# Kernel optimization log

Hardware: AMD Instinct MI355X
Metric: run time of the kernel (lower is better)

## Reference

```python
import jax, jax.numpy as jnp
import numpy as np

S = 1
R = 64
INV_T = 100.0
EVAL_STEPS = 7  # module in eval mode
EPS = 1e-6


def setup_inputs() -> dict:
    key = jax.random.key(0)
    kx, kb = jax.random.split(key)
    B, C, H, W = 8, 512, 64, 64
    x = jax.random.uniform(kx, (B, C, H, W), dtype=jnp.float32)  # non-negative input for NMF
    bases = jax.random.uniform(kb, (B * S, C // S, R), dtype=jnp.float32)
    # F.normalize(bases, dim=1): L2-normalize along D
    bases = bases / jnp.linalg.norm(bases, axis=1, keepdims=True)
    return {"x": x, "bases": bases}


def reference(x, bases):
    B, C, H, W = x.shape
    D = C // S
    N = H * W
    xf = x.reshape(B * S, D, N)  # (BS, D, N)

    # initial coefficients: softmax(inv_t * x^T @ bases)
    coef = jax.nn.softmax(INV_T * jnp.einsum('bdn,bdr->bnr', xf, bases), axis=-1)

    def mu_step(carry, _):
        bases, coef = carry
        # update coef: coef *= (x^T bases) / (coef (bases^T bases) + eps)
        num = jnp.einsum('bdn,bdr->bnr', xf, bases)            # (BS, N, R)
        gram_b = jnp.einsum('bdr,bds->brs', bases, bases)      # (BS, R, R)
        coef = coef * num / (jnp.einsum('bnr,brs->bns', coef, gram_b) + EPS)
        # update bases: bases *= (x coef) / (bases (coef^T coef) + eps)
        num_b = jnp.einsum('bdn,bnr->bdr', xf, coef)           # (BS, D, R)
        gram_c = jnp.einsum('bnr,bns->brs', coef, coef)        # (BS, R, R)
        bases = bases * num_b / (jnp.einsum('bdr,brs->bds', bases, gram_c) + EPS)
        return (bases, coef), None

    (bases, coef), _ = jax.lax.scan(mu_step, (bases, coef), None, length=EVAL_STEPS)

    # compute_coef: one extra coef multiplicative update
    num = jnp.einsum('bdn,bdr->bnr', xf, bases)
    gram_b = jnp.einsum('bdr,bds->brs', bases, bases)
    coef = coef * num / (jnp.einsum('bnr,brs->bns', coef, gram_b) + EPS)

    out = jnp.einsum('bdr,bnr->bdn', bases, coef)  # bases @ coef^T
    return out.reshape(B, C, H, W)
```

## Files before the change

### kernel.cpp

```cpp
#include <hip/hip_runtime.h>
#include <math.h>

#define BATCH 8
#define DD 512
#define NN 4096
#define RR 64
#define NSTEPS 7
#define INV_T 100.0f
#define EPSV 1e-6f
#define GC_SCALE (1.0f / 1024.0f)
#define GC_UNSCALE 1024.0f

typedef __attribute__((ext_vector_type(8))) _Float16 f16x8;
typedef __attribute__((ext_vector_type(4))) _Float16 f16x4;
typedef __attribute__((ext_vector_type(4))) float f32x4;

__device__ __forceinline__ _Float16 f2h(float f) { return (_Float16)f; }

__device__ __forceinline__ void do_xcvt(const float* x, _Float16* x_h,
                                        _Float16* xT_h, int b, int d0, int n0,
                                        int tid, char* smem) {
  _Float16(*t)[72] = (_Float16(*)[72])smem;
  const size_t xbase = (size_t)(b * DD + d0) * NN + n0;
#pragma unroll
  for (int i = 0; i < 4; ++i) {
    const int idx = tid + i * 256;
    const int row = idx >> 4, c4 = (idx & 15) * 4;
    const float4 v = *(const float4*)(x + xbase + (size_t)row * NN + c4);
    f16x4 hv = {f2h(v.x), f2h(v.y), f2h(v.z), f2h(v.w)};
    *(f16x4*)(x_h + xbase + (size_t)row * NN + c4) = hv;
    *(f16x4*)&t[row][c4] = hv;
  }
  __syncthreads();
  const size_t tbase = (size_t)(b * NN + n0) * DD + d0;
#pragma unroll
  for (int i = 0; i < 4; ++i) {
    const int idx = tid + i * 256;
    const int row = idx >> 4, c4 = (idx & 15) * 4;
    f16x4 wv = {t[c4][row], t[c4 + 1][row], t[c4 + 2][row], t[c4 + 3][row]};
    *(f16x4*)(xT_h + tbase + (size_t)row * DD + c4) = wv;
  }
}

__device__ __forceinline__ void do_bases_prep(const float* bin, float* bases32,
                                              _Float16* bases_h,
                                              _Float16* basesT_h, int b, int d0,
                                              int tid, char* smem) {
  float(*t)[65] = (float(*)[65])smem;
  const size_t base = (size_t)(b * DD + d0) * RR;
#pragma unroll
  for (int i = 0; i < 4; ++i) {
    const int idx = tid + i * 256;
    const int row = idx >> 4, c4 = (idx & 15) * 4;
    const float4 v = *(const float4*)(bin + base + row * RR + c4);
    *(float4*)(bases32 + base + row * RR + c4) = v;
    f16x4 hv = {f2h(v.x), f2h(v.y), f2h(v.z), f2h(v.w)};
    *(f16x4*)(bases_h + base + row * RR + c4) = hv;
    t[row][c4] = v.x; t[row][c4 + 1] = v.y; t[row][c4 + 2] = v.z; t[row][c4 + 3] = v.w;
  }
  __syncthreads();
#pragma unroll
  for (int i = 0; i < 4; ++i) {
    const int idx = tid + i * 256;
    const int row = idx >> 4, c4 = (idx & 15) * 4;
    f16x4 wv = {f2h(t[c4][row]), f2h(t[c4 + 1][row]), f2h(t[c4 + 2][row]),
                f2h(t[c4 + 3][row])};
    *(f16x4*)(basesT_h + (size_t)(b * RR + row) * DD + d0 + c4) = wv;
  }
}

__global__ __launch_bounds__(256) void k_gb0(const _Float16* basesT_h,
                                             _Float16* gram_b_h) {
  const int b = blockIdx.x, tid = threadIdx.x;
  const int w = tid >> 6, l = tid & 63, lo = l & 15, hi = l >> 4;
  const _Float16* ap = basesT_h + (size_t)(b * RR + w * 16 + lo) * DD + hi * 8;
  const _Float16* bp = basesT_h + (size_t)(b * RR + lo) * DD + hi * 8;
  f32x4 acc[4] = {};
#pragma unroll
  for (int ks = 0; ks < 16; ++ks) {
    f16x8 a = *(const f16x8*)(ap + ks * 32);
#pragma unroll
    for (int c = 0; c < 4; ++c) {
      f16x8 bb = *(const f16x8*)(bp + (size_t)c * 16 * DD + ks * 32);
      acc[c] = __builtin_amdgcn_mfma_f32_16x16x32_f16(a, bb, acc[c], 0, 0, 0);
    }
  }
  _Float16* op = gram_b_h + (size_t)b * 4096;
#pragma unroll
  for (int c = 0; c < 4; ++c)
#pragma unroll
    for (int r = 0; r < 4; ++r)
      op[(w * 16 + hi * 4 + r) * RR + c * 16 + lo] = f2h(acc[c][r]);
}

__global__ __launch_bounds__(256) void k_gb(const float* pgb,
                                            _Float16* gram_b_h) {
  const int b = blockIdx.x >> 3;
  const int e0 = (blockIdx.x & 7) * 512 + threadIdx.x;
#pragma unroll
  for (int t = 0; t < 2; ++t) {
    const int e = e0 + t * 256;
    float s = 0.f;
#pragma unroll
    for (int sp = 0; sp < 8; ++sp) s += pgb[(size_t)(b * 8 + sp) * 4096 + e];
    gram_b_h[(size_t)b * 4096 + e] = f2h(s);
  }
}

__global__ __launch_bounds__(256) void k_initf(const _Float16* xT_h,
                                               const _Float16* basesT_h,
                                               const _Float16* gram_b_h,
                                               _Float16* coefT_h) {
  __shared__ __attribute__((aligned(16))) _Float16 ct[64][72];
  const int tid = threadIdx.x, w = tid >> 6, l = tid & 63, lo = l & 15,
            hi = l >> 4;
  const int b = blockIdx.x >> 6, n0 = (blockIdx.x & 63) * 64;

  const _Float16* ap = xT_h + (size_t)(b * NN + n0 + w * 16 + lo) * DD + hi * 8;
  const _Float16* bp = basesT_h + (size_t)(b * RR + lo) * DD + hi * 8;
  f32x4 acc[4] = {};
#pragma unroll
  for (int ks = 0; ks < 16; ++ks) {
    f16x8 a = *(const f16x8*)(ap + ks * 32);
#pragma unroll
    for (int c = 0; c < 4; ++c) {
      f16x8 bb = *(const f16x8*)(bp + (size_t)c * 16 * DD + ks * 32);
      acc[c] = __builtin_amdgcn_mfma_f32_16x16x32_f16(a, bb, acc[c], 0, 0, 0);
    }
  }
  float v0[4][4];
#pragma unroll
  for (int reg = 0; reg < 4; ++reg) {
    float m = fmaxf(fmaxf(acc[0][reg], acc[1][reg]),
                    fmaxf(acc[2][reg], acc[3][reg]));
    m = fmaxf(m, __shfl_xor(m, 1));
    m = fmaxf(m, __shfl_xor(m, 2));
    m = fmaxf(m, __shfl_xor(m, 4));
    m = fmaxf(m, __shfl_xor(m, 8));
    float s = 0.f, e[4];
#pragma unroll
    for (int c = 0; c < 4; ++c) {
      e[c] = expf(INV_T * (acc[c][reg] - m));
      s += e[c];
    }
    s += __shfl_xor(s, 1);
    s += __shfl_xor(s, 2);
    s += __shfl_xor(s, 4);
    s += __shfl_xor(s, 8);
    const float inv = 1.f / s;
#pragma unroll
    for (int c = 0; c < 4; ++c) v0[c][reg] = e[c] * inv;
  }
#pragma unroll
  for (int reg = 0; reg < 4; ++reg)
#pragma unroll
    for (int c = 0; c < 4; ++c)
      ct[w * 16 + hi * 4 + reg][c * 16 + lo] = f2h(v0[c][reg]);
  __syncthreads();
  f32x4 den[4] = {};
#pragma unroll
  for (int kk = 0; kk < 2; ++kk) {
    f16x8 a = *(const f16x8*)&ct[w * 16 + lo][kk * 32 + hi * 8];
#pragma unroll
    for (int c = 0; c < 4; ++c) {
      f16x8 gv = *(const f16x8*)(gram_b_h + (size_t)b * 4096 +
                                 (c * 16 + lo) * RR + kk * 32 + hi * 8);
      den[c] = __builtin_amdgcn_mfma_f32_16x16x32_f16(a, gv, den[c], 0, 0, 0);
    }
  }
#pragma unroll
  for (int c = 0; c < 4; ++c) {
    f16x4 t4;
#pragma unroll
    for (int reg = 0; reg < 4; ++reg) {
      const float oldc = (float)ct[w * 16 + hi * 4 + reg][c * 16 + lo];
      t4[reg] = f2h(oldc * acc[c][reg] / (den[c][reg] + EPSV));
    }
    *(f16x4*)(coefT_h + (size_t)(b * RR + c * 16 + lo) * NN + n0 + w * 16 +
              hi * 4) = t4;
  }
}

__device__ __forceinline__ void do_coef1(const _Float16* xT_h,
                                         const _Float16* basesT_h,
                                         const _Float16* gram_b_h,
                                         _Float16* coefT_h, int b, int nt,
                                         int tid, int w, int lo, int hi,
                                         char* smem) {
  _Float16(*ct)[72] = (_Float16(*)[72])smem;
  const int n0 = nt * 64;
#pragma unroll
  for (int i = 0; i < 2; ++i) {
    const int idx = tid + i * 256;
    const int r = idx >> 3, n8 = (idx & 7) * 8;
    f16x8 vv = *(const f16x8*)(coefT_h + (size_t)(b * RR + r) * NN + n0 + n8);
#pragma unroll
    for (int j = 0; j < 8; ++j) ct[n8 + j][r] = vv[j];
  }

  const _Float16* ap = xT_h + (size_t)(b * NN + n0 + w * 16 + lo) * DD + hi * 8;
  const _Float16* bp = basesT_h + (size_t)(b * RR + lo) * DD + hi * 8;
  f32x4 acc[4] = {};
#pragma unroll
  for (int ks = 0; ks < 16; ++ks) {
    f16x8 a = *(const f16x8*)(ap + ks * 32);
#pragma unroll
    for (int c = 0; c < 4; ++c) {
      f16x8 bb = *(const f16x8*)(bp + (size_t)c * 16 * DD + ks * 32);
      acc[c] = __builtin_amdgcn_mfma_f32_16x16x32_f16(a, bb, acc[c], 0, 0, 0);
    }
  }
  __syncthreads();
  f32x4 den[4] = {};
#pragma unroll
  for (int kk = 0; kk < 2; ++kk) {
    f16x8 a = *(const f16x8*)&ct[w * 16 + lo][kk * 32 + hi * 8];
#pragma unroll
    for (int c = 0; c < 4; ++c) {
      f16x8 gv = *(const f16x8*)(gram_b_h + (size_t)b * 4096 +
                                 (c * 16 + lo) * RR + kk * 32 + hi * 8);
      den[c] = __builtin_amdgcn_mfma_f32_16x16x32_f16(a, gv, den[c], 0, 0, 0);
    }
  }
#pragma unroll
  for (int c = 0; c < 4; ++c) {
    f16x4 t4;
#pragma unroll
    for (int reg = 0; reg < 4; ++reg) {
      const float oldc = (float)ct[w * 16 + hi * 4 + reg][c * 16 + lo];
      t4[reg] = f2h(oldc * acc[c][reg] / (den[c][reg] + EPSV));
    }
    *(f16x4*)(coefT_h + (size_t)(b * RR + c * 16 + lo) * NN + n0 + w * 16 +
              hi * 4) = t4;
  }
}

__device__ __forceinline__ void do_numb(const _Float16* x_h,
                                        const _Float16* coefT_h, float* pnb,
                                        int kc, int dt, int b, int w, int lo,
                                        int hi) {
  const _Float16* ap =
      x_h + (size_t)(b * DD + dt * 64 + w * 16 + lo) * NN + kc * 1024 + hi * 8;
  const _Float16* bp = coefT_h + (size_t)(b * RR + lo) * NN + kc * 1024 + hi * 8;
  f32x4 acc[4] = {};
#pragma unroll 4
  for (int ks = 0; ks < 32; ++ks) {
    f16x8 a = *(const f16x8*)(ap + ks * 32);
#pragma unroll
    for (int c = 0; c < 4; ++c) {
      f16x8 bb = *(const f16x8*)(bp + (size_t)c * 16 * NN + ks * 32);
      acc[c] = __builtin_amdgcn_mfma_f32_16x16x32_f16(a, bb, acc[c], 0, 0, 0);
    }
  }
  float* op = pnb + ((size_t)((b * 4 + kc) * DD) + dt * 64 + w * 16 + hi * 4) * RR;
#pragma unroll
  for (int c = 0; c < 4; ++c)
#pragma unroll
    for (int r = 0; r < 4; ++r) op[r * RR + c * 16 + lo] = acc[c][r];
}

__device__ __forceinline__ void do_gramc(const _Float16* coefT_h, float* pgram,
                                         int sp, int b, int w, int lo, int hi) {
  const int k0 = sp * 256;
  const _Float16* ap = coefT_h + (size_t)(b * RR + w * 16 + lo) * NN + k0 + hi * 8;
  const _Float16* bp = coefT_h + (size_t)(b * RR + lo) * NN + k0 + hi * 8;
  f32x4 acc[4] = {};
#pragma unroll
  for (int ks = 0; ks < 8; ++ks) {
    f16x8 a = *(const f16x8*)(ap + ks * 32);
#pragma unroll
    for (int c = 0; c < 4; ++c) {
      f16x8 bb = *(const f16x8*)(bp + (size_t)c * 16 * NN + ks * 32);
      acc[c] = __builtin_amdgcn_mfma_f32_16x16x32_f16(a, bb, acc[c], 0, 0, 0);
    }
  }
  float* op = pgram + ((size_t)(b * 16 + sp) * RR + w * 16 + hi * 4) * RR;
#pragma unroll
  for (int c = 0; c < 4; ++c)
#pragma unroll
    for (int r = 0; r < 4; ++r) op[r * RR + c * 16 + lo] = acc[c][r];
}

__device__ __forceinline__ void do_bases_upd(const float* pnb,
                                             const float* pgram, float* bases32,
                                             _Float16* bases_h,
                                             _Float16* basesT_h, float* pgb,
                                             int dt, int b, int tid, int tx,
                                             int ty, char* smem) {
  float* bsm = (float*)smem;
  _Float16* gsh = (_Float16*)(smem + 16640);
  float* bg = bases32 + (size_t)(b * DD + dt * 64) * RR;
  for (int idx = tid; idx < 4096; idx += 256) {
    const int row = idx >> 6, cc = idx & 63;
    bsm[row * 65 + cc] = bg[row * 64 + cc];
  }
  for (int idx = tid; idx < 4096; idx += 256) {
    float s = 0.f;
#pragma unroll
    for (int sp = 0; sp < 16; ++sp)
      s += pgram[(size_t)(b * 16 + sp) * 4096 + idx];
    gsh[idx] = f2h(s * GC_SCALE);
  }
  __syncthreads();

  float nb[4][4];
#pragma unroll
  for (int i = 0; i < 4; ++i) {
    float4 s = make_float4(0.f, 0.f, 0.f, 0.f);
#pragma unroll
    for (int kc = 0; kc < 4; ++kc) {
      const float4 vv = *(const float4*)(pnb +
          (((size_t)b * 4 + kc) * DD + dt * 64 + ty * 4 + i) * RR + tx * 4);
      s.x += vv.x; s.y += vv.y; s.z += vv.z; s.w += vv.w;
    }
    nb[i][0] = s.x; nb[i][1] = s.y; nb[i][2] = s.z; nb[i][3] = s.w;
  }

  float den[4][4] = {};
  for (int s = 0; s < 64; ++s) {
    float a[4];
#pragma unroll
    for (int i = 0; i < 4; ++i) a[i] = bsm[(ty * 4 + i) * 65 + s];
    const f16x4 gv = *(const f16x4*)&gsh[s * 64 + tx * 4];
    const float g4[4] = {(float)gv[0], (float)gv[1], (float)gv[2], (float)gv[3]};
#pragma unroll
    for (int i = 0; i < 4; ++i)
#pragma unroll
      for (int j = 0; j < 4; ++j) den[i][j] = fmaf(a[i], g4[j], den[i][j]);
  }

  float v[4][4];
#pragma unroll
  for (int i = 0; i < 4; ++i) {
    float4 vv;
#pragma unroll
    for (int j = 0; j < 4; ++j) {
      const float oldb = bsm[(ty * 4 + i) * 65 + tx * 4 + j];
      v[i][j] = oldb * nb[i][j] / fmaf(den[i][j], GC_UNSCALE, EPSV);
    }
    vv.x = v[i][0]; vv.y = v[i][1]; vv.z = v[i][2]; vv.w = v[i][3];
    *(float4*)&bg[(ty * 4 + i) * 64 + tx * 4] = vv;
    f16x4 bv = {f2h(v[i][0]), f2h(v[i][1]), f2h(v[i][2]), f2h(v[i][3])};
    *(f16x4*)(bases_h + (size_t)(b * DD + dt * 64 + ty * 4 + i) * RR + tx * 4) = bv;
  }
#pragma unroll
  for (int j = 0; j < 4; ++j) {
    f16x4 tv = {f2h(v[0][j]), f2h(v[1][j]), f2h(v[2][j]), f2h(v[3][j])};
    *(f16x4*)(basesT_h + (size_t)(b * RR + tx * 4 + j) * DD + dt * 64 + ty * 4) = tv;
  }
  __syncthreads();
#pragma unroll
  for (int i = 0; i < 4; ++i)
#pragma unroll
    for (int j = 0; j < 4; ++j) bsm[(ty * 4 + i) * 65 + tx * 4 + j] = v[i][j];
  __syncthreads();

  float pa[4][4] = {};
  for (int d = 0; d < 64; ++d) {
    float a[4], bb[4];
#pragma unroll
    for (int i = 0; i < 4; ++i) a[i] = bsm[d * 65 + ty * 4 + i];
#pragma unroll
    for (int j = 0; j < 4; ++j) bb[j] = bsm[d * 65 + tx * 4 + j];
#pragma unroll
    for (int i = 0; i < 4; ++i)
#pragma unroll
      for (int j = 0; j < 4; ++j) pa[i][j] = fmaf(a[i], bb[j], pa[i][j]);
  }
  float* pp = pgb + (size_t)(b * 8 + dt) * 4096;
#pragma unroll
  for (int i = 0; i < 4; ++i) {
    float4 vv = make_float4(pa[i][0], pa[i][1], pa[i][2], pa[i][3]);
    *(float4*)(pp + (ty * 4 + i) * 64 + tx * 4) = vv;
  }
}

__global__ __launch_bounds__(256) void k_cout(const _Float16* xT_h,
                                              const _Float16* basesT_h,
                                              const _Float16* gram_b_h,
                                              const _Float16* coefT_h,
                                              const _Float16* bases_h,
                                              float* out) {
  __shared__ __attribute__((aligned(16))) _Float16 ct[64][72];
  const int tid = threadIdx.x, w = tid >> 6, l = tid & 63, lo = l & 15,
            hi = l >> 4;
  const int b = blockIdx.x >> 6, n0 = (blockIdx.x & 63) * 64;

#pragma unroll
  for (int i = 0; i < 2; ++i) {
    const int idx = tid + i * 256;
    const int r = idx >> 3, n8 = (idx & 7) * 8;
    f16x8 vv = *(const f16x8*)(coefT_h + (size_t)(b * RR + r) * NN + n0 + n8);
#pragma unroll
    for (int j = 0; j < 8; ++j) ct[n8 + j][r] = vv[j];
  }

  const _Float16* ap = xT_h + (size_t)(b * NN + n0 + w * 16 + lo) * DD + hi * 8;
  const _Float16* bp = basesT_h + (size_t)(b * RR + lo) * DD + hi * 8;
  f32x4 acc[4] = {};
#pragma unroll
  for (int ks = 0; ks < 16; ++ks) {
    f16x8 a = *(const f16x8*)(ap + ks * 32);
#pragma unroll
    for (int c = 0; c < 4; ++c) {
      f16x8 bb = *(const f16x8*)(bp + (size_t)c * 16 * DD + ks * 32);
      acc[c] = __builtin_amdgcn_mfma_f32_16x16x32_f16(a, bb, acc[c], 0, 0, 0);
    }
  }
  __syncthreads();
  f32x4 den[4] = {};
#pragma unroll
  for (int kk = 0; kk < 2; ++kk) {
    f16x8 a = *(const f16x8*)&ct[w * 16 + lo][kk * 32 + hi * 8];
#pragma unroll
    for (int c = 0; c < 4; ++c) {
      f16x8 gv = *(const f16x8*)(gram_b_h + (size_t)b * 4096 +
                                 (c * 16 + lo) * RR + kk * 32 + hi * 8);
      den[c] = __builtin_amdgcn_mfma_f32_16x16x32_f16(a, gv, den[c], 0, 0, 0);
    }
  }
  float v[4][4];
#pragma unroll
  for (int c = 0; c < 4; ++c)
#pragma unroll
    for (int reg = 0; reg < 4; ++reg) {
      const float oldc = (float)ct[w * 16 + hi * 4 + reg][c * 16 + lo];
      v[c][reg] = oldc * acc[c][reg] / (den[c][reg] + EPSV);
    }
  __syncthreads();
#pragma unroll
  for (int c = 0; c < 4; ++c)
#pragma unroll
    for (int reg = 0; reg < 4; ++reg)
      ct[w * 16 + hi * 4 + reg][c * 16 + lo] = f2h(v[c][reg]);
  __syncthreads();

  for (int dt = 0; dt < 8; ++dt) {
    const _Float16* bap =
        bases_h + (size_t)(b * DD + dt * 64 + w * 16 + lo) * RR + hi * 8;
    f32x4 oacc[4] = {};
#pragma unroll
    for (int kk = 0; kk < 2; ++kk) {
      f16x8 a = *(const f16x8*)(bap + kk * 32);
#pragma unroll
      for (int c = 0; c < 4; ++c) {
        f16x8 bb = *(const f16x8*)&ct[c * 16 + lo][kk * 32 + hi * 8];
        oacc[c] = __builtin_amdgcn_mfma_f32_16x16x32_f16(a, bb, oacc[c], 0, 0, 0);
      }
    }
    float* op = out + (size_t)(b * DD + dt * 64 + w * 16 + hi * 4) * NN + n0;
#pragma unroll
    for (int c = 0; c < 4; ++c)
#pragma unroll
      for (int r = 0; r < 4; ++r) op[(size_t)r * NN + c * 16 + lo] = oacc[c][r];
  }
}

__global__ __launch_bounds__(256) void k_out(const _Float16* bases_h,
                                             const _Float16* coefT_h,
                                             float* out) {
  __shared__ __attribute__((aligned(16))) _Float16 ct[64][72];
  const int tid = threadIdx.x, w = tid >> 6, l = tid & 63, lo = l & 15,
            hi = l >> 4;
  const int nt = blockIdx.x, dt = blockIdx.y, b = blockIdx.z;
  const int n0 = nt * 64;
#pragma unroll
  for (int i = 0; i < 2; ++i) {
    const int idx = tid + i * 256;
    const int r = idx >> 3, n8 = (idx & 7) * 8;
    f16x8 vv = *(const f16x8*)(coefT_h + (size_t)(b * RR + r) * NN + n0 + n8);
#pragma unroll
    for (int j = 0; j < 8; ++j) ct[n8 + j][r] = vv[j];
  }
  __syncthreads();
  const _Float16* ap =
      bases_h + (size_t)(b * DD + dt * 64 + w * 16 + lo) * RR + hi * 8;
  f32x4 acc[4] = {};
#pragma unroll
  for (int kk = 0; kk < 2; ++kk) {
    f16x8 a = *(const f16x8*)(ap + kk * 32);
#pragma unroll
    for (int c = 0; c < 4; ++c) {
      f16x8 bb = *(const f16x8*)&ct[c * 16 + lo][kk * 32 + hi * 8];
      acc[c] = __builtin_amdgcn_mfma_f32_16x16x32_f16(a, bb, acc[c], 0, 0, 0);
    }
  }
  float* op = out + (size_t)(b * DD + dt * 64 + w * 16 + hi * 4) * NN + n0;
#pragma unroll
  for (int c = 0; c < 4; ++c)
#pragma unroll
    for (int r = 0; r < 4; ++r) op[(size_t)r * NN + c * 16 + lo] = acc[c][r];
}

__global__ __launch_bounds__(256) void k_prep(const float* x, const float* bin,
                                              float* b32, _Float16* x_h,
                                              _Float16* xT_h, _Float16* bh,
                                              _Float16* bth) {
  __shared__ __attribute__((aligned(16))) char smem[16640];
  const int g = blockIdx.x, tid = threadIdx.x;
  if (g < 4096)
    do_xcvt(x, x_h, xT_h, g >> 9, ((g >> 6) & 7) * 64, (g & 63) * 64, tid, smem);
  else {
    const int q = g - 4096;
    do_bases_prep(bin, b32, bh, bth, q >> 3, (q & 7) * 64, tid, smem);
  }
}
__global__ __launch_bounds__(256) void k_coef1(const _Float16* xT_h,
                                               const _Float16* basesT_h,
                                               const _Float16* gram_b_h,
                                               _Float16* coefT_h) {
  __shared__ __attribute__((aligned(16))) char smem[9216];
  const int tid = threadIdx.x, w = tid >> 6, l = tid & 63, lo = l & 15,
            hi = l >> 4;
  do_coef1(xT_h, basesT_h, gram_b_h, coefT_h, blockIdx.x >> 6, blockIdx.x & 63,
           tid, w, lo, hi, smem);
}
__global__ __launch_bounds__(256) void k_nbgc(const _Float16* x_h,
                                              const _Float16* coefT_h,
                                              float* pnb, float* pgram) {
  const int tid = threadIdx.x, w = tid >> 6, l = tid & 63, lo = l & 15,
            hi = l >> 4;
  const int g = blockIdx.x;
  if (g < 256)
    do_numb(x_h, coefT_h, pnb, g & 3, (g >> 2) & 7, g >> 5, w, lo, hi);
  else {
    const int q = g - 256;
    do_gramc(coefT_h, pgram, q & 15, q >> 4, w, lo, hi);
  }
}
__global__ __launch_bounds__(256) void k_bupd(const float* pnb,
                                              const float* pgram, float* b32,
                                              _Float16* bh, _Float16* bth,
                                              float* pgb) {
  __shared__ __attribute__((aligned(16))) char smem[24832];
  do_bases_upd(pnb, pgram, b32, bh, bth, pgb, blockIdx.x & 7, blockIdx.x >> 3,
               threadIdx.x, threadIdx.x & 15, threadIdx.x >> 4, smem);
}

extern "C" void kernel_launch(void* const* d_in, const int* in_sizes, int n_in,
                              void* d_out, int out_size, void* d_ws,
                              size_t ws_size, hipStream_t stream) {
  (void)in_sizes; (void)n_in; (void)out_size;
  const float* x = (const float*)d_in[0];
  const float* bin = (const float*)d_in[1];
  float* W = (float*)d_ws;
  float* O = (float*)d_out;

  float* bases32 = W;
  float* pnb = bases32 + 262144;
  float* pgram = pnb + 1048576;
  float* pgb = pgram + 524288;
  _Float16* coefT_h = (_Float16*)(pgb + 262144);
  _Float16* bases_h = coefT_h + 2097152;
  _Float16* basesT_h = bases_h + 262144;
  _Float16* gram_b_h = basesT_h + 262144;
  _Float16* ws_end = gram_b_h + 32768;

  const size_t xhalves = (size_t)BATCH * NN * DD;
  const size_t need = ((char*)(ws_end + 2 * xhalves)) - (char*)W;
  _Float16* xT_h;
  _Float16* x_h;
  const bool ws_fits = (ws_size >= need);
  if (ws_fits) {
    xT_h = ws_end;
    x_h = xT_h + xhalves;
  } else {
    xT_h = (_Float16*)O;
    x_h = xT_h + xhalves;
  }

  k_prep<<<4160, 256, 0, stream>>>(x, bin, bases32, x_h, xT_h, bases_h,
                                   basesT_h);
  k_gb0<<<BATCH, 256, 0, stream>>>(basesT_h, gram_b_h);
  k_initf<<<512, 256, 0, stream>>>(xT_h, basesT_h, gram_b_h, coefT_h);
  for (int s = 0; s < NSTEPS; ++s) {
    k_nbgc<<<384, 256, 0, stream>>>(x_h, coefT_h, pnb, pgram);
    k_bupd<<<64, 256, 0, stream>>>(pnb, pgram, bases32, bases_h, basesT_h, pgb);
    k_gb<<<64, 256, 0, stream>>>(pgb, gram_b_h);
    if (s < NSTEPS - 1)
      k_coef1<<<512, 256, 0, stream>>>(xT_h, basesT_h, gram_b_h, coefT_h);
  }
  if (ws_fits) {
    k_cout<<<512, 256, 0, stream>>>(xT_h, basesT_h, gram_b_h, coefT_h, bases_h,
                                    O);
  } else {
    k_coef1<<<512, 256, 0, stream>>>(xT_h, basesT_h, gram_b_h, coefT_h);
    k_out<<<dim3(64, 8, BATCH), 256, 0, stream>>>(bases_h, coefT_h, O);
  }
}
```

Before: 524.5 us.

## Fuse coef Gram partials into coef-update kernels and interleave batch block mapping

The coefficient Gram matrix (coef^T coef) is now computed per 64-column tile inside k_initf and k_coef1 from the freshly updated coefficients held in shared memory. This removes the separate gram_c blocks that re-read coefT from global memory. As a result k_bupd must reduce 64 partials per batch instead of 16, which it does with float4 loads, and the pgram buffer grows four times. Block indices are also remapped so batch is the fastest-varying dimension, spreading batches across CUs.

```diff
diff --git a/kernel.cpp b/kernel.cpp
--- a/kernel.cpp
+++ b/kernel.cpp
@@ -95,8 +95,8 @@
 
 __global__ __launch_bounds__(256) void k_gb(const float* pgb,
                                             _Float16* gram_b_h) {
-  const int b = blockIdx.x >> 3;
-  const int e0 = (blockIdx.x & 7) * 512 + threadIdx.x;
+  const int b = blockIdx.x & 7;
+  const int e0 = (blockIdx.x >> 3) * 512 + threadIdx.x;
 #pragma unroll
   for (int t = 0; t < 2; ++t) {
     const int e = e0 + t * 256;
@@ -107,14 +107,36 @@
   }
 }
 
+__device__ __forceinline__ void emit_gram(const _Float16 (*ctT)[72],
+                                          float* pgram, int b, int nt, int w,
+                                          int lo, int hi) {
+  f32x4 ga[4] = {};
+#pragma unroll
+  for (int kk = 0; kk < 2; ++kk) {
+    f16x8 a = *(const f16x8*)&ctT[w * 16 + lo][kk * 32 + hi * 8];
+#pragma unroll
+    for (int c = 0; c < 4; ++c) {
+      f16x8 bb = *(const f16x8*)&ctT[c * 16 + lo][kk * 32 + hi * 8];
+      ga[c] = __builtin_amdgcn_mfma_f32_16x16x32_f16(a, bb, ga[c], 0, 0, 0);
+    }
+  }
+  float* gp = pgram + ((size_t)(b * 64 + nt) * RR + w * 16 + hi * 4) * RR;
+#pragma unroll
+  for (int c = 0; c < 4; ++c)
+#pragma unroll
+    for (int r = 0; r < 4; ++r) gp[r * RR + c * 16 + lo] = ga[c][r];
+}
+
 __global__ __launch_bounds__(256) void k_initf(const _Float16* xT_h,
                                                const _Float16* basesT_h,
                                                const _Float16* gram_b_h,
-                                               _Float16* coefT_h) {
+                                               _Float16* coefT_h,
+                                               float* pgram) {
   __shared__ __attribute__((aligned(16))) _Float16 ct[64][72];
+  __shared__ __attribute__((aligned(16))) _Float16 ctT[64][72];
   const int tid = threadIdx.x, w = tid >> 6, l = tid & 63, lo = l & 15,
             hi = l >> 4;
-  const int b = blockIdx.x >> 6, n0 = (blockIdx.x & 63) * 64;
+  const int b = blockIdx.x & 7, nt = blockIdx.x >> 3, n0 = nt * 64;
 
   const _Float16* ap = xT_h + (size_t)(b * NN + n0 + w * 16 + lo) * DD + hi * 8;
   const _Float16* bp = basesT_h + (size_t)(b * RR + lo) * DD + hi * 8;
@@ -174,21 +196,28 @@
 #pragma unroll
     for (int reg = 0; reg < 4; ++reg) {
       const float oldc = (float)ct[w * 16 + hi * 4 + reg][c * 16 + lo];
-      t4[reg] = f2h(oldc * acc[c][reg] / (den[c][reg] + EPSV));
+      const _Float16 nh = f2h(oldc * acc[c][reg] / (den[c][reg] + EPSV));
+      t4[reg] = nh;
+      ctT[c * 16 + lo][w * 16 + hi * 4 + reg] = nh;
     }
     *(f16x4*)(coefT_h + (size_t)(b * RR + c * 16 + lo) * NN + n0 + w * 16 +
               hi * 4) = t4;
   }
-}
-
-__device__ __forceinline__ void do_coef1(const _Float16* xT_h,
-                                         const _Float16* basesT_h,
-                                         const _Float16* gram_b_h,
-                                         _Float16* coefT_h, int b, int nt,
-                                         int tid, int w, int lo, int hi,
-                                         char* smem) {
-  _Float16(*ct)[72] = (_Float16(*)[72])smem;
-  const int n0 = nt * 64;
+  __syncthreads();
+  emit_gram(ctT, pgram, b, nt, w, lo, hi);
+}
+
+__global__ __launch_bounds__(256) void k_coef1(const _Float16* xT_h,
+                                               const _Float16* basesT_h,
+                                               const _Float16* gram_b_h,
+                                               _Float16* coefT_h,
+                                               float* pgram) {
+  __shared__ __attribute__((aligned(16))) _Float16 ct[64][72];
+  __shared__ __attribute__((aligned(16))) _Float16 ctT[64][72];
+  const int tid = threadIdx.x, w = tid >> 6, l = tid & 63, lo = l & 15,
+            hi = l >> 4;
+  const int b = blockIdx.x & 7, nt = blockIdx.x >> 3, n0 = nt * 64;
+
 #pragma unroll
   for (int i = 0; i < 2; ++i) {
     const int idx = tid + i * 256;
@@ -228,17 +257,25 @@
 #pragma unroll
     for (int reg = 0; reg < 4; ++reg) {
       const float oldc = (float)ct[w * 16 + hi * 4 + reg][c * 16 + lo];
-      t4[reg] = f2h(oldc * acc[c][reg] / (den[c][reg] + EPSV));
+      const _Float16 nh = f2h(oldc * acc[c][reg] / (den[c][reg] + EPSV));
+      t4[reg] = nh;
+      ctT[c * 16 + lo][w * 16 + hi * 4 + reg] = nh;
     }
     *(f16x4*)(coefT_h + (size_t)(b * RR + c * 16 + lo) * NN + n0 + w * 16 +
               hi * 4) = t4;
   }
-}
-
-__device__ __forceinline__ void do_numb(const _Float16* x_h,
-                                        const _Float16* coefT_h, float* pnb,
-                                        int kc, int dt, int b, int w, int lo,
-                                        int hi) {
+  __syncthreads();
+  emit_gram(ctT, pgram, b, nt, w, lo, hi);
+}
+
+__global__ __launch_bounds__(256) void k_numb(const _Float16* x_h,
+                                              const _Float16* coefT_h,
+                                              float* pnb) {
+  const int tid = threadIdx.x, w = tid >> 6, l = tid & 63, lo = l & 15,
+            hi = l >> 4;
+  const int b = blockIdx.x & 7;
+  const int q = blockIdx.x >> 3;
+  const int dt = q & 7, kc = q >> 3;
   const _Float16* ap =
       x_h + (size_t)(b * DD + dt * 64 + w * 16 + lo) * NN + kc * 1024 + hi * 8;
   const _Float16* bp = coefT_h + (size_t)(b * RR + lo) * NN + kc * 1024 + hi * 8;
@@ -259,47 +296,32 @@
     for (int r = 0; r < 4; ++r) op[r * RR + c * 16 + lo] = acc[c][r];
 }
 
-__device__ __forceinline__ void do_gramc(const _Float16* coefT_h, float* pgram,
-                                         int sp, int b, int w, int lo, int hi) {
-  const int k0 = sp * 256;
-  const _Float16* ap = coefT_h + (size_t)(b * RR + w * 16 + lo) * NN + k0 + hi * 8;
-  const _Float16* bp = coefT_h + (size_t)(b * RR + lo) * NN + k0 + hi * 8;
-  f32x4 acc[4] = {};
-#pragma unroll
-  for (int ks = 0; ks < 8; ++ks) {
-    f16x8 a = *(const f16x8*)(ap + ks * 32);
-#pragma unroll
-    for (int c = 0; c < 4; ++c) {
-      f16x8 bb = *(const f16x8*)(bp + (size_t)c * 16 * NN + ks * 32);
-      acc[c] = __builtin_amdgcn_mfma_f32_16x16x32_f16(a, bb, acc[c], 0, 0, 0);
-    }
-  }
-  float* op = pgram + ((size_t)(b * 16 + sp) * RR + w * 16 + hi * 4) * RR;
-#pragma unroll
-  for (int c = 0; c < 4; ++c)
-#pragma unroll
-    for (int r = 0; r < 4; ++r) op[r * RR + c * 16 + lo] = acc[c][r];
-}
-
-__device__ __forceinline__ void do_bases_upd(const float* pnb,
-                                             const float* pgram, float* bases32,
-                                             _Float16* bases_h,
-                                             _Float16* basesT_h, float* pgb,
-                                             int dt, int b, int tid, int tx,
-                                             int ty, char* smem) {
+__global__ __launch_bounds__(256) void k_bupd(const float* pnb,
+                                              const float* pgram, float* b32,
+                                              _Float16* bases_h,
+                                              _Float16* basesT_h, float* pgb) {
+  __shared__ __attribute__((aligned(16))) char smem[24832];
   float* bsm = (float*)smem;
   _Float16* gsh = (_Float16*)(smem + 16640);
-  float* bg = bases32 + (size_t)(b * DD + dt * 64) * RR;
+  const int tid = threadIdx.x, tx = tid & 15, ty = tid >> 4;
+  const int b = blockIdx.x & 7, dt = blockIdx.x >> 3;
+  float* bg = b32 + (size_t)(b * DD + dt * 64) * RR;
   for (int idx = tid; idx < 4096; idx += 256) {
     const int row = idx >> 6, cc = idx & 63;
     bsm[row * 65 + cc] = bg[row * 64 + cc];
   }
-  for (int idx = tid; idx < 4096; idx += 256) {
-    float s = 0.f;
-#pragma unroll
-    for (int sp = 0; sp < 16; ++sp)
-      s += pgram[(size_t)(b * 16 + sp) * 4096 + idx];
-    gsh[idx] = f2h(s * GC_SCALE);
+#pragma unroll
+  for (int q = 0; q < 4; ++q) {
+    const int e = q * 1024 + tid * 4;
+    float4 s = make_float4(0.f, 0.f, 0.f, 0.f);
+    for (int sp = 0; sp < 64; ++sp) {
+      const float4 vv = *(const float4*)(pgram + (size_t)(b * 64 + sp) * 4096 + e);
+      s.x += vv.x; s.y += vv.y; s.z += vv.z; s.w += vv.w;
+    }
+    gsh[e + 0] = f2h(s.x * GC_SCALE);
+    gsh[e + 1] = f2h(s.y * GC_SCALE);
+    gsh[e + 2] = f2h(s.z * GC_SCALE);
+    gsh[e + 3] = f2h(s.w * GC_SCALE);
   }
   __syncthreads();
 
@@ -384,7 +406,7 @@
   __shared__ __attribute__((aligned(16))) _Float16 ct[64][72];
   const int tid = threadIdx.x, w = tid >> 6, l = tid & 63, lo = l & 15,
             hi = l >> 4;
-  const int b = blockIdx.x >> 6, n0 = (blockIdx.x & 63) * 64;
+  const int b = blockIdx.x & 7, n0 = (blockIdx.x >> 3) * 64;
 
 #pragma unroll
   for (int i = 0; i < 2; ++i) {
@@ -505,37 +527,6 @@
     do_bases_prep(bin, b32, bh, bth, q >> 3, (q & 7) * 64, tid, smem);
   }
 }
-__global__ __launch_bounds__(256) void k_coef1(const _Float16* xT_h,
-                                               const _Float16* basesT_h,
-                                               const _Float16* gram_b_h,
-                                               _Float16* coefT_h) {
-  __shared__ __attribute__((aligned(16))) char smem[9216];
-  const int tid = threadIdx.x, w = tid >> 6, l = tid & 63, lo = l & 15,
-            hi = l >> 4;
-  do_coef1(xT_h, basesT_h, gram_b_h, coefT_h, blockIdx.x >> 6, blockIdx.x & 63,
-           tid, w, lo, hi, smem);
-}
-__global__ __launch_bounds__(256) void k_nbgc(const _Float16* x_h,
-                                              const _Float16* coefT_h,
-                                              float* pnb, float* pgram) {
-  const int tid = threadIdx.x, w = tid >> 6, l = tid & 63, lo = l & 15,
-            hi = l >> 4;
-  const int g = blockIdx.x;
-  if (g < 256)
-    do_numb(x_h, coefT_h, pnb, g & 3, (g >> 2) & 7, g >> 5, w, lo, hi);
-  else {
-    const int q = g - 256;
-    do_gramc(coefT_h, pgram, q & 15, q >> 4, w, lo, hi);
-  }
-}
-__global__ __launch_bounds__(256) void k_bupd(const float* pnb,
-                                              const float* pgram, float* b32,
-                                              _Float16* bh, _Float16* bth,
-                                              float* pgb) {
-  __shared__ __attribute__((aligned(16))) char smem[24832];
-  do_bases_upd(pnb, pgram, b32, bh, bth, pgb, blockIdx.x & 7, blockIdx.x >> 3,
-               threadIdx.x, threadIdx.x & 15, threadIdx.x >> 4, smem);
-}
 
 extern "C" void kernel_launch(void* const* d_in, const int* in_sizes, int n_in,
                               void* d_out, int out_size, void* d_ws,
@@ -549,7 +540,7 @@
   float* bases32 = W;
   float* pnb = bases32 + 262144;
   float* pgram = pnb + 1048576;
-  float* pgb = pgram + 524288;
+  float* pgb = pgram + 2097152;
   _Float16* coefT_h = (_Float16*)(pgb + 262144);
   _Float16* bases_h = coefT_h + 2097152;
   _Float16* basesT_h = bases_h + 262144;
@@ -572,19 +563,20 @@
   k_prep<<<4160, 256, 0, stream>>>(x, bin, bases32, x_h, xT_h, bases_h,
                                    basesT_h);
   k_gb0<<<BATCH, 256, 0, stream>>>(basesT_h, gram_b_h);
-  k_initf<<<512, 256, 0, stream>>>(xT_h, basesT_h, gram_b_h, coefT_h);
+  k_initf<<<512, 256, 0, stream>>>(xT_h, basesT_h, gram_b_h, coefT_h, pgram);
   for (int s = 0; s < NSTEPS; ++s) {
-    k_nbgc<<<384, 256, 0, stream>>>(x_h, coefT_h, pnb, pgram);
+    k_numb<<<256, 256, 0, stream>>>(x_h, coefT_h, pnb);
     k_bupd<<<64, 256, 0, stream>>>(pnb, pgram, bases32, bases_h, basesT_h, pgb);
     k_gb<<<64, 256, 0, stream>>>(pgb, gram_b_h);
     if (s < NSTEPS - 1)
-      k_coef1<<<512, 256, 0, stream>>>(xT_h, basesT_h, gram_b_h, coefT_h);
+      k_coef1<<<512, 256, 0, stream>>>(xT_h, basesT_h, gram_b_h, coefT_h,
+                                       pgram);
   }
   if (ws_fits) {
     k_cout<<<512, 256, 0, stream>>>(xT_h, basesT_h, gram_b_h, coefT_h, bases_h,
                                     O);
   } else {
-    k_coef1<<<512, 256, 0, stream>>>(xT_h, basesT_h, gram_b_h, coefT_h);
+    k_coef1<<<512, 256, 0, stream>>>(xT_h, basesT_h, gram_b_h, coefT_h, pgram);
     k_out<<<dim3(64, 8, BATCH), 256, 0, stream>>>(bases_h, coefT_h, O);
   }
 }
```

New measurement: 541.6 us. +3.3%, slower.

## Split K across waves and shrink tiles to raise grid parallelism in NMF kernels

Applied to the files above, without the earlier changes.

The coef-update, init and output kernels now work on 32-column tiles, with pairs of waves splitting the 512-long D reduction and combining partial sums through shared memory. This doubles the block count to fill the GPU better. The num_b kernel splits N into 16 chunks instead of 4, giving 1024 blocks plus gram blocks, and the bases update sums more partials from a larger workspace. Block indices are reordered so batch is the fastest-varying index. The trade-offs are extra shared-memory reductions and syncs, half-idle waves in the epilogue, and more partial-sum traffic through global memory.

```diff
diff --git a/kernel.cpp b/kernel.cpp
--- a/kernel.cpp
+++ b/kernel.cpp
@@ -95,8 +95,8 @@
 
 __global__ __launch_bounds__(256) void k_gb(const float* pgb,
                                             _Float16* gram_b_h) {
-  const int b = blockIdx.x >> 3;
-  const int e0 = (blockIdx.x & 7) * 512 + threadIdx.x;
+  const int b = blockIdx.x & 7;
+  const int e0 = (blockIdx.x >> 3) * 512 + threadIdx.x;
 #pragma unroll
   for (int t = 0; t < 2; ++t) {
     const int e = e0 + t * 256;
@@ -111,16 +111,20 @@
                                                const _Float16* basesT_h,
                                                const _Float16* gram_b_h,
                                                _Float16* coefT_h) {
-  __shared__ __attribute__((aligned(16))) _Float16 ct[64][72];
+  __shared__ __attribute__((aligned(16))) float red[16][2][64];
+  __shared__ __attribute__((aligned(16))) _Float16 ct[32][72];
   const int tid = threadIdx.x, w = tid >> 6, l = tid & 63, lo = l & 15,
             hi = l >> 4;
-  const int b = blockIdx.x >> 6, n0 = (blockIdx.x & 63) * 64;
-
-  const _Float16* ap = xT_h + (size_t)(b * NN + n0 + w * 16 + lo) * DD + hi * 8;
-  const _Float16* bp = basesT_h + (size_t)(b * RR + lo) * DD + hi * 8;
+  const int nsub = w >> 1, khalf = w & 1;
+  const int b = blockIdx.x & 7, n0 = (blockIdx.x >> 3) * 32;
+
+  const _Float16* ap = xT_h + (size_t)(b * NN + n0 + nsub * 16 + lo) * DD +
+                       khalf * 256 + hi * 8;
+  const _Float16* bp =
+      basesT_h + (size_t)(b * RR + lo) * DD + khalf * 256 + hi * 8;
   f32x4 acc[4] = {};
 #pragma unroll
-  for (int ks = 0; ks < 16; ++ks) {
+  for (int ks = 0; ks < 8; ++ks) {
     f16x8 a = *(const f16x8*)(ap + ks * 32);
 #pragma unroll
     for (int c = 0; c < 4; ++c) {
@@ -128,81 +132,95 @@
       acc[c] = __builtin_amdgcn_mfma_f32_16x16x32_f16(a, bb, acc[c], 0, 0, 0);
     }
   }
-  float v0[4][4];
-#pragma unroll
-  for (int reg = 0; reg < 4; ++reg) {
-    float m = fmaxf(fmaxf(acc[0][reg], acc[1][reg]),
-                    fmaxf(acc[2][reg], acc[3][reg]));
-    m = fmaxf(m, __shfl_xor(m, 1));
-    m = fmaxf(m, __shfl_xor(m, 2));
-    m = fmaxf(m, __shfl_xor(m, 4));
-    m = fmaxf(m, __shfl_xor(m, 8));
-    float s = 0.f, e[4];
-#pragma unroll
-    for (int c = 0; c < 4; ++c) {
-      e[c] = expf(INV_T * (acc[c][reg] - m));
-      s += e[c];
-    }
-    s += __shfl_xor(s, 1);
-    s += __shfl_xor(s, 2);
-    s += __shfl_xor(s, 4);
-    s += __shfl_xor(s, 8);
-    const float inv = 1.f / s;
-#pragma unroll
-    for (int c = 0; c < 4; ++c) v0[c][reg] = e[c] * inv;
-  }
-#pragma unroll
-  for (int reg = 0; reg < 4; ++reg)
-#pragma unroll
-    for (int c = 0; c < 4; ++c)
-      ct[w * 16 + hi * 4 + reg][c * 16 + lo] = f2h(v0[c][reg]);
-  __syncthreads();
-  f32x4 den[4] = {};
-#pragma unroll
-  for (int kk = 0; kk < 2; ++kk) {
-    f16x8 a = *(const f16x8*)&ct[w * 16 + lo][kk * 32 + hi * 8];
-#pragma unroll
-    for (int c = 0; c < 4; ++c) {
-      f16x8 gv = *(const f16x8*)(gram_b_h + (size_t)b * 4096 +
-                                 (c * 16 + lo) * RR + kk * 32 + hi * 8);
-      den[c] = __builtin_amdgcn_mfma_f32_16x16x32_f16(a, gv, den[c], 0, 0, 0);
-    }
-  }
-#pragma unroll
-  for (int c = 0; c < 4; ++c) {
-    f16x4 t4;
+  if (khalf) {
+#pragma unroll
+    for (int c = 0; c < 4; ++c)
+#pragma unroll
+      for (int reg = 0; reg < 4; ++reg) red[c * 4 + reg][nsub][l] = acc[c][reg];
+  }
+  __syncthreads();
+  if (!khalf) {
+#pragma unroll
+    for (int c = 0; c < 4; ++c)
+#pragma unroll
+      for (int reg = 0; reg < 4; ++reg)
+        acc[c][reg] += red[c * 4 + reg][nsub][l];
 #pragma unroll
     for (int reg = 0; reg < 4; ++reg) {
-      const float oldc = (float)ct[w * 16 + hi * 4 + reg][c * 16 + lo];
-      t4[reg] = f2h(oldc * acc[c][reg] / (den[c][reg] + EPSV));
-    }
-    *(f16x4*)(coefT_h + (size_t)(b * RR + c * 16 + lo) * NN + n0 + w * 16 +
-              hi * 4) = t4;
-  }
-}
-
-__device__ __forceinline__ void do_coef1(const _Float16* xT_h,
-                                         const _Float16* basesT_h,
-                                         const _Float16* gram_b_h,
-                                         _Float16* coefT_h, int b, int nt,
-                                         int tid, int w, int lo, int hi,
-                                         char* smem) {
-  _Float16(*ct)[72] = (_Float16(*)[72])smem;
-  const int n0 = nt * 64;
-#pragma unroll
-  for (int i = 0; i < 2; ++i) {
-    const int idx = tid + i * 256;
-    const int r = idx >> 3, n8 = (idx & 7) * 8;
+      float m = fmaxf(fmaxf(acc[0][reg], acc[1][reg]),
+                      fmaxf(acc[2][reg], acc[3][reg]));
+      m = fmaxf(m, __shfl_xor(m, 1));
+      m = fmaxf(m, __shfl_xor(m, 2));
+      m = fmaxf(m, __shfl_xor(m, 4));
+      m = fmaxf(m, __shfl_xor(m, 8));
+      float s = 0.f, e[4];
+#pragma unroll
+      for (int c = 0; c < 4; ++c) {
+        e[c] = expf(INV_T * (acc[c][reg] - m));
+        s += e[c];
+      }
+      s += __shfl_xor(s, 1);
+      s += __shfl_xor(s, 2);
+      s += __shfl_xor(s, 4);
+      s += __shfl_xor(s, 8);
+      const float inv = 1.f / s;
+#pragma unroll
+      for (int c = 0; c < 4; ++c)
+        ct[nsub * 16 + hi * 4 + reg][c * 16 + lo] = f2h(e[c] * inv);
+    }
+  }
+  __syncthreads();
+  if (!khalf) {
+    f32x4 den[4] = {};
+#pragma unroll
+    for (int kk = 0; kk < 2; ++kk) {
+      f16x8 a = *(const f16x8*)&ct[nsub * 16 + lo][kk * 32 + hi * 8];
+#pragma unroll
+      for (int c = 0; c < 4; ++c) {
+        f16x8 gv = *(const f16x8*)(gram_b_h + (size_t)b * 4096 +
+                                   (c * 16 + lo) * RR + kk * 32 + hi * 8);
+        den[c] = __builtin_amdgcn_mfma_f32_16x16x32_f16(a, gv, den[c], 0, 0, 0);
+      }
+    }
+#pragma unroll
+    for (int c = 0; c < 4; ++c) {
+      f16x4 t4;
+#pragma unroll
+      for (int reg = 0; reg < 4; ++reg) {
+        const float oldc = (float)ct[nsub * 16 + hi * 4 + reg][c * 16 + lo];
+        t4[reg] = f2h(oldc * acc[c][reg] / (den[c][reg] + EPSV));
+      }
+      *(f16x4*)(coefT_h + (size_t)(b * RR + c * 16 + lo) * NN + n0 + nsub * 16 +
+                hi * 4) = t4;
+    }
+  }
+}
+
+__global__ __launch_bounds__(256) void k_coef1(const _Float16* xT_h,
+                                               const _Float16* basesT_h,
+                                               const _Float16* gram_b_h,
+                                               _Float16* coefT_h) {
+  __shared__ __attribute__((aligned(16))) float red[16][2][64];
+  __shared__ __attribute__((aligned(16))) _Float16 ct[32][72];
+  const int tid = threadIdx.x, w = tid >> 6, l = tid & 63, lo = l & 15,
+            hi = l >> 4;
+  const int nsub = w >> 1, khalf = w & 1;
+  const int b = blockIdx.x & 7, n0 = (blockIdx.x >> 3) * 32;
+
+  {
+    const int r = tid >> 2, n8 = (tid & 3) * 8;
     f16x8 vv = *(const f16x8*)(coefT_h + (size_t)(b * RR + r) * NN + n0 + n8);
 #pragma unroll
     for (int j = 0; j < 8; ++j) ct[n8 + j][r] = vv[j];
   }
 
-  const _Float16* ap = xT_h + (size_t)(b * NN + n0 + w * 16 + lo) * DD + hi * 8;
-  const _Float16* bp = basesT_h + (size_t)(b * RR + lo) * DD + hi * 8;
+  const _Float16* ap = xT_h + (size_t)(b * NN + n0 + nsub * 16 + lo) * DD +
+                       khalf * 256 + hi * 8;
+  const _Float16* bp =
+      basesT_h + (size_t)(b * RR + lo) * DD + khalf * 256 + hi * 8;
   f32x4 acc[4] = {};
 #pragma unroll
-  for (int ks = 0; ks < 16; ++ks) {
+  for (int ks = 0; ks < 8; ++ks) {
     f16x8 a = *(const f16x8*)(ap + ks * 32);
 #pragma unroll
     for (int c = 0; c < 4; ++c) {
@@ -210,53 +228,42 @@
       acc[c] = __builtin_amdgcn_mfma_f32_16x16x32_f16(a, bb, acc[c], 0, 0, 0);
     }
   }
-  __syncthreads();
-  f32x4 den[4] = {};
-#pragma unroll
-  for (int kk = 0; kk < 2; ++kk) {
-    f16x8 a = *(const f16x8*)&ct[w * 16 + lo][kk * 32 + hi * 8];
-#pragma unroll
-    for (int c = 0; c < 4; ++c) {
-      f16x8 gv = *(const f16x8*)(gram_b_h + (size_t)b * 4096 +
-                                 (c * 16 + lo) * RR + kk * 32 + hi * 8);
-      den[c] = __builtin_amdgcn_mfma_f32_16x16x32_f16(a, gv, den[c], 0, 0, 0);
-    }
-  }
-#pragma unroll
-  for (int c = 0; c < 4; ++c) {
-    f16x4 t4;
-#pragma unroll
-    for (int reg = 0; reg < 4; ++reg) {
-      const float oldc = (float)ct[w * 16 + hi * 4 + reg][c * 16 + lo];
-      t4[reg] = f2h(oldc * acc[c][reg] / (den[c][reg] + EPSV));
-    }
-    *(f16x4*)(coefT_h + (size_t)(b * RR + c * 16 + lo) * NN + n0 + w * 16 +
-              hi * 4) = t4;
-  }
-}
-
-__device__ __forceinline__ void do_numb(const _Float16* x_h,
-                                        const _Float16* coefT_h, float* pnb,
-                                        int kc, int dt, int b, int w, int lo,
-                                        int hi) {
-  const _Float16* ap =
-      x_h + (size_t)(b * DD + dt * 64 + w * 16 + lo) * NN + kc * 1024 + hi * 8;
-  const _Float16* bp = coefT_h + (size_t)(b * RR + lo) * NN + kc * 1024 + hi * 8;
-  f32x4 acc[4] = {};
-#pragma unroll 4
-  for (int ks = 0; ks < 32; ++ks) {
-    f16x8 a = *(const f16x8*)(ap + ks * 32);
-#pragma unroll
-    for (int c = 0; c < 4; ++c) {
-      f16x8 bb = *(const f16x8*)(bp + (size_t)c * 16 * NN + ks * 32);
-      acc[c] = __builtin_amdgcn_mfma_f32_16x16x32_f16(a, bb, acc[c], 0, 0, 0);
-    }
-  }
-  float* op = pnb + ((size_t)((b * 4 + kc) * DD) + dt * 64 + w * 16 + hi * 4) * RR;
-#pragma unroll
-  for (int c = 0; c < 4; ++c)
-#pragma unroll
-    for (int r = 0; r < 4; ++r) op[r * RR + c * 16 + lo] = acc[c][r];
+  if (khalf) {
+#pragma unroll
+    for (int c = 0; c < 4; ++c)
+#pragma unroll
+      for (int reg = 0; reg < 4; ++reg) red[c * 4 + reg][nsub][l] = acc[c][reg];
+  }
+  __syncthreads();
+  if (!khalf) {
+#pragma unroll
+    for (int c = 0; c < 4; ++c)
+#pragma unroll
+      for (int reg = 0; reg < 4; ++reg)
+        acc[c][reg] += red[c * 4 + reg][nsub][l];
+    f32x4 den[4] = {};
+#pragma unroll
+    for (int kk = 0; kk < 2; ++kk) {
+      f16x8 a = *(const f16x8*)&ct[nsub * 16 + lo][kk * 32 + hi * 8];
+#pragma unroll
+      for (int c = 0; c < 4; ++c) {
+        f16x8 gv = *(const f16x8*)(gram_b_h + (size_t)b * 4096 +
+                                   (c * 16 + lo) * RR + kk * 32 + hi * 8);
+        den[c] = __builtin_amdgcn_mfma_f32_16x16x32_f16(a, gv, den[c], 0, 0, 0);
+      }
+    }
+#pragma unroll
+    for (int c = 0; c < 4; ++c) {
+      f16x4 t4;
+#pragma unroll
+      for (int reg = 0; reg < 4; ++reg) {
+        const float oldc = (float)ct[nsub * 16 + hi * 4 + reg][c * 16 + lo];
+        t4[reg] = f2h(oldc * acc[c][reg] / (den[c][reg] + EPSV));
+      }
+      *(f16x4*)(coefT_h + (size_t)(b * RR + c * 16 + lo) * NN + n0 + nsub * 16 +
+                hi * 4) = t4;
+    }
+  }
 }
 
 __device__ __forceinline__ void do_gramc(const _Float16* coefT_h, float* pgram,
@@ -281,15 +288,51 @@
     for (int r = 0; r < 4; ++r) op[r * RR + c * 16 + lo] = acc[c][r];
 }
 
-__device__ __forceinline__ void do_bases_upd(const float* pnb,
-                                             const float* pgram, float* bases32,
-                                             _Float16* bases_h,
-                                             _Float16* basesT_h, float* pgb,
-                                             int dt, int b, int tid, int tx,
-                                             int ty, char* smem) {
+__global__ __launch_bounds__(256) void k_nbgc(const _Float16* x_h,
+                                              const _Float16* coefT_h,
+                                              float* pnb, float* pgram) {
+  const int tid = threadIdx.x, w = tid >> 6, l = tid & 63, lo = l & 15,
+            hi = l >> 4;
+  const int g = blockIdx.x;
+  if (g < 1024) {
+    const int b = g & 7, q = g >> 3;
+    const int dt = q & 7, kc = q >> 3;
+    const _Float16* ap =
+        x_h + (size_t)(b * DD + dt * 64 + w * 16 + lo) * NN + kc * 256 + hi * 8;
+    const _Float16* bp =
+        coefT_h + (size_t)(b * RR + lo) * NN + kc * 256 + hi * 8;
+    f32x4 acc[4] = {};
+#pragma unroll
+    for (int ks = 0; ks < 8; ++ks) {
+      f16x8 a = *(const f16x8*)(ap + ks * 32);
+#pragma unroll
+      for (int c = 0; c < 4; ++c) {
+        f16x8 bb = *(const f16x8*)(bp + (size_t)c * 16 * NN + ks * 32);
+        acc[c] = __builtin_amdgcn_mfma_f32_16x16x32_f16(a, bb, acc[c], 0, 0, 0);
+      }
+    }
+    float* op =
+        pnb + ((size_t)((b * 16 + kc) * DD) + dt * 64 + w * 16 + hi * 4) * RR;
+#pragma unroll
+    for (int c = 0; c < 4; ++c)
+#pragma unroll
+      for (int r = 0; r < 4; ++r) op[r * RR + c * 16 + lo] = acc[c][r];
+  } else {
+    const int q = g - 1024;
+    do_gramc(coefT_h, pgram, q & 15, q >> 4, w, lo, hi);
+  }
+}
+
+__global__ __launch_bounds__(256) void k_bupd(const float* pnb,
+                                              const float* pgram, float* b32,
+                                              _Float16* bases_h,
+                                              _Float16* basesT_h, float* pgb) {
+  __shared__ __attribute__((aligned(16))) char smem[24832];
   float* bsm = (float*)smem;
   _Float16* gsh = (_Float16*)(smem + 16640);
-  float* bg = bases32 + (size_t)(b * DD + dt * 64) * RR;
+  const int tid = threadIdx.x, tx = tid & 15, ty = tid >> 4;
+  const int b = blockIdx.x & 7, dt = blockIdx.x >> 3;
+  float* bg = b32 + (size_t)(b * DD + dt * 64) * RR;
   for (int idx = tid; idx < 4096; idx += 256) {
     const int row = idx >> 6, cc = idx & 63;
     bsm[row * 65 + cc] = bg[row * 64 + cc];
@@ -308,9 +351,9 @@
   for (int i = 0; i < 4; ++i) {
     float4 s = make_float4(0.f, 0.f, 0.f, 0.f);
 #pragma unroll
-    for (int kc = 0; kc < 4; ++kc) {
+    for (int kc = 0; kc < 16; ++kc) {
       const float4 vv = *(const float4*)(pnb +
-          (((size_t)b * 4 + kc) * DD + dt * 64 + ty * 4 + i) * RR + tx * 4);
+          (((size_t)b * 16 + kc) * DD + dt * 64 + ty * 4 + i) * RR + tx * 4);
       s.x += vv.x; s.y += vv.y; s.z += vv.z; s.w += vv.w;
     }
     nb[i][0] = s.x; nb[i][1] = s.y; nb[i][2] = s.z; nb[i][3] = s.w;
@@ -381,25 +424,27 @@
                                               const _Float16* coefT_h,
                                               const _Float16* bases_h,
                                               float* out) {
-  __shared__ __attribute__((aligned(16))) _Float16 ct[64][72];
+  __shared__ __attribute__((aligned(16))) float red[16][2][64];
+  __shared__ __attribute__((aligned(16))) _Float16 ct[32][72];
   const int tid = threadIdx.x, w = tid >> 6, l = tid & 63, lo = l & 15,
             hi = l >> 4;
-  const int b = blockIdx.x >> 6, n0 = (blockIdx.x & 63) * 64;
-
-#pragma unroll
-  for (int i = 0; i < 2; ++i) {
-    const int idx = tid + i * 256;
-    const int r = idx >> 3, n8 = (idx & 7) * 8;
+  const int nsub = w >> 1, khalf = w & 1;
+  const int b = blockIdx.x & 7, n0 = (blockIdx.x >> 3) * 32;
+
+  {
+    const int r = tid >> 2, n8 = (tid & 3) * 8;
     f16x8 vv = *(const f16x8*)(coefT_h + (size_t)(b * RR + r) * NN + n0 + n8);
 #pragma unroll
     for (int j = 0; j < 8; ++j) ct[n8 + j][r] = vv[j];
   }
 
-  const _Float16* ap = xT_h + (size_t)(b * NN + n0 + w * 16 + lo) * DD + hi * 8;
-  const _Float16* bp = basesT_h + (size_t)(b * RR + lo) * DD + hi * 8;
+  const _Float16* ap = xT_h + (size_t)(b * NN + n0 + nsub * 16 + lo) * DD +
+                       khalf * 256 + hi * 8;
+  const _Float16* bp =
+      basesT_h + (size_t)(b * RR + lo) * DD + khalf * 256 + hi * 8;
   f32x4 acc[4] = {};
 #pragma unroll
-  for (int ks = 0; ks < 16; ++ks) {
+  for (int ks = 0; ks < 8; ++ks) {
     f16x8 a = *(const f16x8*)(ap + ks * 32);
 #pragma unroll
     for (int c = 0; c < 4; ++c) {
@@ -407,50 +452,57 @@
       acc[c] = __builtin_amdgcn_mfma_f32_16x16x32_f16(a, bb, acc[c], 0, 0, 0);
     }
   }
-  __syncthreads();
-  f32x4 den[4] = {};
-#pragma unroll
-  for (int kk = 0; kk < 2; ++kk) {
-    f16x8 a = *(const f16x8*)&ct[w * 16 + lo][kk * 32 + hi * 8];
-#pragma unroll
-    for (int c = 0; c < 4; ++c) {
-      f16x8 gv = *(const f16x8*)(gram_b_h + (size_t)b * 4096 +
-                                 (c * 16 + lo) * RR + kk * 32 + hi * 8);
-      den[c] = __builtin_amdgcn_mfma_f32_16x16x32_f16(a, gv, den[c], 0, 0, 0);
-    }
-  }
-  float v[4][4];
-#pragma unroll
-  for (int c = 0; c < 4; ++c)
-#pragma unroll
-    for (int reg = 0; reg < 4; ++reg) {
-      const float oldc = (float)ct[w * 16 + hi * 4 + reg][c * 16 + lo];
-      v[c][reg] = oldc * acc[c][reg] / (den[c][reg] + EPSV);
-    }
-  __syncthreads();
-#pragma unroll
-  for (int c = 0; c < 4; ++c)
-#pragma unroll
-    for (int reg = 0; reg < 4; ++reg)
-      ct[w * 16 + hi * 4 + reg][c * 16 + lo] = f2h(v[c][reg]);
+  if (khalf) {
+#pragma unroll
+    for (int c = 0; c < 4; ++c)
+#pragma unroll
+      for (int reg = 0; reg < 4; ++reg) red[c * 4 + reg][nsub][l] = acc[c][reg];
+  }
+  __syncthreads();
+  if (!khalf) {
+#pragma unroll
+    for (int c = 0; c < 4; ++c)
+#pragma unroll
+      for (int reg = 0; reg < 4; ++reg)
+        acc[c][reg] += red[c * 4 + reg][nsub][l];
+    f32x4 den[4] = {};
+#pragma unroll
+    for (int kk = 0; kk < 2; ++kk) {
+      f16x8 a = *(const f16x8*)&ct[nsub * 16 + lo][kk * 32 + hi * 8];
+#pragma unroll
+      for (int c = 0; c < 4; ++c) {
+        f16x8 gv = *(const f16x8*)(gram_b_h + (size_t)b * 4096 +
+                                   (c * 16 + lo) * RR + kk * 32 + hi * 8);
+        den[c] = __builtin_amdgcn_mfma_f32_16x16x32_f16(a, gv, den[c], 0, 0, 0);
+      }
+    }
+#pragma unroll
+    for (int c = 0; c < 4; ++c)
+#pragma unroll
+      for (int reg = 0; reg < 4; ++reg) {
+        const float oldc = (float)ct[nsub * 16 + hi * 4 + reg][c * 16 + lo];
+        ct[nsub * 16 + hi * 4 + reg][c * 16 + lo] =
+            f2h(oldc * acc[c][reg] / (den[c][reg] + EPSV));
+      }
+  }
   __syncthreads();
 
   for (int dt = 0; dt < 8; ++dt) {
     const _Float16* bap =
         bases_h + (size_t)(b * DD + dt * 64 + w * 16 + lo) * RR + hi * 8;
-    f32x4 oacc[4] = {};
+    f32x4 oacc[2] = {};
 #pragma unroll
     for (int kk = 0; kk < 2; ++kk) {
       f16x8 a = *(const f16x8*)(bap + kk * 32);
 #pragma unroll
-      for (int c = 0; c < 4; ++c) {
+      for (int c = 0; c < 2; ++c) {
         f16x8 bb = *(const f16x8*)&ct[c * 16 + lo][kk * 32 + hi * 8];
         oacc[c] = __builtin_amdgcn_mfma_f32_16x16x32_f16(a, bb, oacc[c], 0, 0, 0);
       }
     }
     float* op = out + (size_t)(b * DD + dt * 64 + w * 16 + hi * 4) * NN + n0;
 #pragma unroll
-    for (int c = 0; c < 4; ++c)
+    for (int c = 0; c < 2; ++c)
 #pragma unroll
       for (int r = 0; r < 4; ++r) op[(size_t)r * NN + c * 16 + lo] = oacc[c][r];
   }
@@ -505,37 +557,6 @@
     do_bases_prep(bin, b32, bh, bth, q >> 3, (q & 7) * 64, tid, smem);
   }
 }
-__global__ __launch_bounds__(256) void k_coef1(const _Float16* xT_h,
-                                               const _Float16* basesT_h,
-                                               const _Float16* gram_b_h,
-                                               _Float16* coefT_h) {
-  __shared__ __attribute__((aligned(16))) char smem[9216];
-  const int tid = threadIdx.x, w = tid >> 6, l = tid & 63, lo = l & 15,
-            hi = l >> 4;
-  do_coef1(xT_h, basesT_h, gram_b_h, coefT_h, blockIdx.x >> 6, blockIdx.x & 63,
-           tid, w, lo, hi, smem);
-}
-__global__ __launch_bounds__(256) void k_nbgc(const _Float16* x_h,
-                                              const _Float16* coefT_h,
-                                              float* pnb, float* pgram) {
-  const int tid = threadIdx.x, w = tid >> 6, l = tid & 63, lo = l & 15,
-            hi = l >> 4;
-  const int g = blockIdx.x;
-  if (g < 256)
-    do_numb(x_h, coefT_h, pnb, g & 3, (g >> 2) & 7, g >> 5, w, lo, hi);
-  else {
-    const int q = g - 256;
-    do_gramc(coefT_h, pgram, q & 15, q >> 4, w, lo, hi);
-  }
-}
-__global__ __launch_bounds__(256) void k_bupd(const float* pnb,
-                                              const float* pgram, float* b32,
-                                              _Float16* bh, _Float16* bth,
-                                              float* pgb) {
-  __shared__ __attribute__((aligned(16))) char smem[24832];
-  do_bases_upd(pnb, pgram, b32, bh, bth, pgb, blockIdx.x & 7, blockIdx.x >> 3,
-               threadIdx.x, threadIdx.x & 15, threadIdx.x >> 4, smem);
-}
 
 extern "C" void kernel_launch(void* const* d_in, const int* in_sizes, int n_in,
                               void* d_out, int out_size, void* d_ws,
@@ -548,7 +569,7 @@
 
   float* bases32 = W;
   float* pnb = bases32 + 262144;
-  float* pgram = pnb + 1048576;
+  float* pgram = pnb + 4194304;
   float* pgb = pgram + 524288;
   _Float16* coefT_h = (_Float16*)(pgb + 262144);
   _Float16* bases_h = coefT_h + 2097152;
@@ -572,19 +593,19 @@
   k_prep<<<4160, 256, 0, stream>>>(x, bin, bases32, x_h, xT_h, bases_h,
                                    basesT_h);
   k_gb0<<<BATCH, 256, 0, stream>>>(basesT_h, gram_b_h);
-  k_initf<<<512, 256, 0, stream>>>(xT_h, basesT_h, gram_b_h, coefT_h);
+  k_initf<<<1024, 256, 0, stream>>>(xT_h, basesT_h, gram_b_h, coefT_h);
   for (int s = 0; s < NSTEPS; ++s) {
-    k_nbgc<<<384, 256, 0, stream>>>(x_h, coefT_h, pnb, pgram);
+    k_nbgc<<<1152, 256, 0, stream>>>(x_h, coefT_h, pnb, pgram);
     k_bupd<<<64, 256, 0, stream>>>(pnb, pgram, bases32, bases_h, basesT_h, pgb);
     k_gb<<<64, 256, 0, stream>>>(pgb, gram_b_h);
     if (s < NSTEPS - 1)
-      k_coef1<<<512, 256, 0, stream>>>(xT_h, basesT_h, gram_b_h, coefT_h);
+      k_coef1<<<1024, 256, 0, stream>>>(xT_h, basesT_h, gram_b_h, coefT_h);
   }
   if (ws_fits) {
-    k_cout<<<512, 256, 0, stream>>>(xT_h, basesT_h, gram_b_h, coefT_h, bases_h,
-                                    O);
+    k_cout<<<1024, 256, 0, stream>>>(xT_h, basesT_h, gram_b_h, coefT_h,
+                                     bases_h, O);
   } else {
-    k_coef1<<<512, 256, 0, stream>>>(xT_h, basesT_h, gram_b_h, coefT_h);
+    k_coef1<<<1024, 256, 0, stream>>>(xT_h, basesT_h, gram_b_h, coefT_h);
     k_out<<<dim3(64, 8, BATCH), 256, 0, stream>>>(bases_h, coefT_h, O);
   }
 }
```

Measured after the change: 567.2 us. 1.08x slower.
